# Performance work log

Measured on AMD Instinct MI355X. Metric: run time of the kernel, lower is better.

## Reference

```python
import jax, jax.numpy as jnp
import numpy as np

BATCH = 8192
N_BANDS = 2000
TARGET = 500
FIRST_HIDDEN = 50
LEAKY_SLOPE = 0.01  # torch LeakyReLU default


def _tridiag_solve(lower, diag, upper, rhs):
    """Thomas algorithm. lower/upper: (n-1,), diag: (n,), rhs: (n, B). Returns (n, B)."""
    dt = rhs.dtype
    up = jnp.concatenate([upper, jnp.zeros((1,), dt)])   # (n,)
    lo = jnp.concatenate([jnp.zeros((1,), dt), lower])   # (n,)

    def fwd(carry, inp):
        cp_prev, dp_prev = carry
        d_i, u_i, l_i, r_i = inp
        m = d_i - l_i * cp_prev
        cp = u_i / m
        dp = (r_i - l_i * dp_prev) / m
        return (cp, dp), (cp, dp)

    init = (jnp.zeros((), dt), jnp.zeros(rhs.shape[1:], dt))
    _, (cps, dps) = jax.lax.scan(fwd, init, (diag, up, lo, rhs))

    def bwd(x_next, inp):
        cp, dp = inp
        x = dp - cp * x_next
        return x, x

    _, xs = jax.lax.scan(bwd, jnp.zeros(rhs.shape[1:], dt), (cps, dps), reverse=True)
    return xs


def natural_cubic_spline_coeffs(times, path):
    """times: (n,), path: (B, n) -> (a, b, two_c, three_d), each (B, n-1)."""
    h = times[1:] - times[:-1]            # (n-1,)
    hr = 1.0 / h
    hr2 = hr * hr
    diffs3 = 3.0 * (path[:, 1:] - path[:, :-1])   # (B, n-1)
    diffs6 = 2.0 * diffs3
    pds = diffs3 * hr2                             # (B, n-1)
    n = path.shape[1]
    diag = (jnp.zeros((n,), path.dtype).at[:-1].set(hr).at[1:].add(hr)) * 2.0
    rhs = jnp.zeros_like(path).at[:, :-1].set(pds).at[:, 1:].add(pds)  # (B, n)
    kd = _tridiag_solve(hr, diag, hr, rhs.T).T     # knot derivatives (B, n)
    a = path[:, :-1]
    b = kd[:, :-1]
    two_c = (diffs6 * hr - 4.0 * kd[:, :-1] - 2.0 * kd[:, 1:]) * hr
    three_d = (-diffs6 * hr + 3.0 * (kd[:, :-1] + kd[:, 1:])) * hr2
    return a, b, two_c, three_d


def spline_evaluate(times, coeffs, t):
    """Evaluate at points t: (T,). Returns (B, T)."""
    a, b, two_c, three_d = coeffs
    idx = jnp.clip(jnp.searchsorted(times, t, side='left') - 1, 0, times.shape[0] - 2)
    frac = t - times[idx]                  # (T,)
    inner = 0.5 * two_c[:, idx] + three_d[:, idx] * frac / 3.0
    inner = b[:, idx] + inner * frac
    return a[:, idx] + inner * frac


def leaky_relu(x):
    return jnp.where(x >= 0, x, LEAKY_SLOPE * x)


def setup_inputs() -> dict:
    key = jax.random.key(0)
    ks = jax.random.split(key, 8)
    return {
        'x': jax.random.uniform(ks[0], (BATCH, N_BANDS), dtype=jnp.float32),
        'raw_index': jax.random.normal(ks[1], (TARGET,), dtype=jnp.float32),
        'W1': jax.random.normal(ks[2], (TARGET, FIRST_HIDDEN), dtype=jnp.float32) * 0.05,
        'b1': jax.random.normal(ks[3], (FIRST_HIDDEN,), dtype=jnp.float32) * 0.05,
        'W2': jax.random.normal(ks[4], (FIRST_HIDDEN, 10), dtype=jnp.float32) * 0.1,
        'b2': jax.random.normal(ks[5], (10,), dtype=jnp.float32) * 0.1,
        'W3': jax.random.normal(ks[6], (10, 1), dtype=jnp.float32) * 0.1,
        'b3': jax.random.normal(ks[7], (1,), dtype=jnp.float32) * 0.1,
    }


def reference(x, raw_index, W1, b1, W2, b2, W3, b3):
    # x: (B, n_bands). Spline is fit along the band axis with knots linspace(0,1,n_bands).
    times = jnp.linspace(0.0, 1.0, x.shape[1]).astype(x.dtype)
    coeffs = natural_cubic_spline_coeffs(times, x)
    # Each BandIndex machine evaluates the spline at sigmoid(raw_index_i) -> batched over all i.
    t_eval = jax.nn.sigmoid(raw_index)             # (T,)
    outputs = spline_evaluate(times, coeffs, t_eval)  # (B, T)
    h = leaky_relu(outputs @ W1 + b1)
    h = leaky_relu(h @ W2 + b2)
    soc_hat = (h @ W3 + b3).reshape(-1)            # (B,)
    return soc_hat
```

## Files before the change

kernel.cpp:

```cpp
#include <hip/hip_runtime.h>

#define NB 2000
#define BATCH 8192
#define NT 500
#define NH1 50
#define NH2 10
#define HRc 1999.0f
#define STEPc (1.0f/1999.0f)
#define LP 520

typedef __attribute__((ext_vector_type(8))) short short8;
typedef __attribute__((ext_vector_type(4))) float f32x4;

__device__ __forceinline__ float b2f(unsigned short u) {
    return __uint_as_float(((unsigned int)u) << 16);
}
__device__ __forceinline__ unsigned short f2b(float f) {
    unsigned int u = __float_as_uint(f);
    return (unsigned short)((u + 0x7FFFu + ((u >> 16) & 1u)) >> 16);
}
__device__ __forceinline__ float ldv(const void* p, int i, int flag) {
    return flag ? b2f(((const unsigned short*)p)[i]) : ((const float*)p)[i];
}
__device__ __forceinline__ int wave_detect(const void* x) {
    const unsigned char* xb = (const unsigned char*)x;
    int lane = threadIdx.x & 63;
    int pred = xb[4 * lane + 1] > 0x3F;
    unsigned long long m = __ballot(pred);
    return (__popcll(m) > 4) ? 0 : 1;
}

__global__ __launch_bounds__(64, 1) void p1_stencil(
        const void* __restrict__ xdet, const void* __restrict__ raw_index,
        float* __restrict__ S_coef, int* __restrict__ S_base) {
    __shared__ float cp_tab[64];
    __shared__ float sc[2];
    int tid = threadIdx.x;
    int flag = wave_detect(xdet);
    if (tid == 0) {
        double cp = 0.5;
        cp_tab[0] = 0.5f;
        for (int i = 1; i < 64; ++i) { cp = 1.0 / (4.0 - cp); cp_tab[i] = (float)cp; }
        sc[0] = (float)cp;
        sc[1] = (float)(1.0 / (2.0 - cp));
    }
    __syncthreads();
    int t = blockIdx.x * 64 + tid;
    if (t >= NT) return;
    float c_inf = sc[0], w_last = sc[1];

    float coef_rel[34];
    #pragma unroll
    for (int k = 0; k < 34; ++k) coef_rel[k] = 0.0f;

    float r = ldv(raw_index, t, flag);
    float v = 1.0f / (1.0f + expf(-r));
    int lo = 0, hi = NB;
    while (lo < hi) {
        int mid = (lo + hi) >> 1;
        float tm = (float)mid * STEPc;
        if (tm < v) lo = mid + 1; else hi = mid;
    }
    int idx = lo - 1;
    idx = idx < 0 ? 0 : (idx > NB - 2 ? NB - 2 : idx);
    float f = v - (float)idx * STEPc;
    float u = f * HRc;
    float A = 1.0f + u * u * (2.0f * u - 3.0f);
    float B = u * u * (3.0f - 2.0f * u);
    float C = f * (1.0f - u) * (1.0f - u);
    float D = f * u * (u - 1.0f);

    const float g3 = 3.0f * HRc * HRc;
    const float invhr = 1.0f / HRc;

    #pragma unroll
    for (int row = 0; row < 2; ++row) {
        int j = idx + row;
        float scale = row ? D : C;
        float z[35];
        #pragma unroll
        for (int q = 0; q < 35; ++q) z[q] = 0.0f;
        float w0 = (j <= NB - 2) ? ((j < 64) ? cp_tab[j] : c_inf) : w_last;
        z[17] = w0 * invhr;
        #pragma unroll
        for (int s = 1; s <= 17; ++s) {
            int m = j + s;
            float wm;
            if (m <= NB - 2)      wm = (m < 64) ? cp_tab[m] : c_inf;
            else if (m == NB - 1) wm = w_last;
            else                  wm = 0.0f;
            z[17 + s] = -wm * z[17 + s - 1];
        }
        #pragma unroll
        for (int s = 16; s >= -17; --s) {
            int m = j + s;
            float cpv;
            if (m >= NB - 1 || m < 0) cpv = 0.0f;
            else                      cpv = (m < 64) ? cp_tab[m] : c_inf;
            z[17 + s] = z[17 + s] - cpv * z[17 + s + 1];
        }
        #pragma unroll
        for (int s = -16; s <= 16; ++s) {
            int m = j + s;
            float gv = 0.0f;
            if (m >= 1)      gv += z[17 + s - 1];
            if (m <= NB - 2) gv -= z[17 + s + 1];
            if (m == NB - 1) gv += z[17 + s];
            if (m == 0)      gv -= z[17 + s];
            gv *= g3;
            bool valid = (m >= 0) && (m <= NB - 1);
            coef_rel[s + row + 16] += valid ? scale * gv : 0.0f;
        }
    }
    coef_rel[16] += A;
    coef_rel[17] += B;

    #pragma unroll
    for (int j = 0; j < 34; ++j) S_coef[t * 34 + j] = coef_rel[j];
    S_base[t] = idx;
}

__global__ __launch_bounds__(256) void m_build(
        const void* __restrict__ xdet, const void* __restrict__ W1,
        const float* __restrict__ S_coef, const int* __restrict__ S_base,
        unsigned int* __restrict__ MB) {
    __shared__ int sb[NT];
    int tid = threadIdx.x;
    int flag = wave_detect(xdet);
    for (int i = tid; i < NT; i += 256) sb[i] = S_base[i];
    __syncthreads();
    int k2 = blockIdx.x * 4 + (tid >> 6);
    int h = tid & 63;
    int hh = h < NH1 ? h : NH1 - 1;
    int k0 = 2 * k2;
    float acc0 = 0.0f, acc1 = 0.0f;
    if (k0 < NB) {
        #pragma unroll 4
        for (int t = 0; t < NT; ++t) {
            int idx = sb[t];
            int rel0 = k0 - idx + 16;
            if (rel0 >= -1 && rel0 < 34) {
                float w1v = ldv(W1, t * NH1 + hh, flag);
                if (rel0 >= 0)  acc0 += S_coef[t * 34 + rel0] * w1v;
                if (rel0 < 33)  acc1 += S_coef[t * 34 + rel0 + 1] * w1v;
            }
        }
    }
    bool ok = (h < NH1) && (k0 < NB);
    unsigned int lo16 = ok ? (unsigned int)f2b(acc0) : 0u;
    unsigned int hi16 = ok ? (unsigned int)f2b(acc1) : 0u;
    int kt = k0 >> 5;
    int kr = k0 & 31;
    int gg = kr >> 3;
    int j  = kr & 7;
    int ht = h >> 4;
    int lt = gg * 16 + (h & 15);
    MB[(((kt * 4 + ht) * 64 + lt) << 2) + (j >> 1)] = lo16 | (hi16 << 16);
}

__global__ __launch_bounds__(512, 4) void g_fused(
        const void* __restrict__ x, const unsigned int* __restrict__ MB,
        const void* __restrict__ b1, const void* __restrict__ W2,
        const void* __restrict__ b2, const void* __restrict__ W3,
        const void* __restrict__ b3, void* __restrict__ out) {
    __shared__ __align__(16) unsigned short lx[2][16 * LP];
    __shared__ float red[8][16][68];
    __shared__ float Wmlp[NH1 * NH2 + NH1 + NH2 + NH2 + 1];

    int tid = threadIdx.x;
    int flag = wave_detect(x);

    for (int i = tid; i < NH1 * NH2; i += 512) Wmlp[i] = ldv(W2, i, flag);
    if (tid < NH1) Wmlp[500 + tid] = ldv(b1, tid, flag);
    if (tid < NH2) Wmlp[550 + tid] = ldv(b2, tid, flag);
    if (tid < NH2) Wmlp[560 + tid] = ldv(W3, tid, flag);
    if (tid == 0)  Wmlp[570] = ldv(b3, 0, flag);

    int lane = tid & 63;
    int c16  = tid & 15;
    int g    = (tid >> 4) & 3;
    int w    = tid >> 6;
    int srow = tid >> 5;
    int soff = tid & 31;
    int r0   = blockIdx.x * 16;
    const unsigned short* xs = (const unsigned short*)x;
    const float*          xf = (const float*)x;
    size_t crow = (size_t)(r0 + srow) * NB;

    f32x4 acc[4];
    #pragma unroll
    for (int ht = 0; ht < 4; ++ht) acc[ht] = (f32x4){0.f, 0.f, 0.f, 0.f};

    union AU { uint4 u; short8 s; };
    const uint4* mb4 = (const uint4*)MB;

    #define LDSEG(dst, gk) do {                                           \
        int _gk = (gk);                                                   \
        if (_gk + 8 <= NB) {                                              \
            if (flag) {                                                   \
                (dst) = *(const uint4*)(xs + crow + _gk);                 \
            } else {                                                      \
                float4 _v0 = *(const float4*)(xf + crow + _gk);           \
                float4 _v1 = *(const float4*)(xf + crow + _gk + 4);       \
                (dst).x = (unsigned)f2b(_v0.x) | ((unsigned)f2b(_v0.y) << 16); \
                (dst).y = (unsigned)f2b(_v0.z) | ((unsigned)f2b(_v0.w) << 16); \
                (dst).z = (unsigned)f2b(_v1.x) | ((unsigned)f2b(_v1.y) << 16); \
                (dst).w = (unsigned)f2b(_v1.z) | ((unsigned)f2b(_v1.w) << 16); \
            }                                                             \
        } else {                                                          \
            (dst) = make_uint4(0u, 0u, 0u, 0u);                           \
        }                                                                 \
    } while (0)

    {
        uint4 p0, p1;
        LDSEG(p0, soff * 8);
        LDSEG(p1, soff * 8 + 256);
        *(uint4*)&lx[0][srow * LP + soff * 8]       = p0;
        *(uint4*)&lx[0][srow * LP + soff * 8 + 256] = p1;
    }

    int cur = 0;
    #pragma unroll
    for (int c = 0; c < 4; ++c) {
        __syncthreads();
        uint4 s0 = make_uint4(0u,0u,0u,0u), s1 = make_uint4(0u,0u,0u,0u);
        if (c < 3) {
            LDSEG(s0, (c + 1) * 512 + soff * 8);
            LDSEG(s1, (c + 1) * 512 + soff * 8 + 256);
        }
        #pragma unroll
        for (int dk = 0; dk < 2; ++dk) {
            int ktl = 2 * w + dk;
            AU a;
            a.u = *(const uint4*)&lx[cur][c16 * LP + ktl * 32 + g * 8];
            int kt = c * 16 + ktl;
            #pragma unroll
            for (int ht = 0; ht < 4; ++ht) {
                AU b; b.u = mb4[(kt * 4 + ht) * 64 + lane];
                acc[ht] = __builtin_amdgcn_mfma_f32_16x16x32_bf16(a.s, b.s, acc[ht], 0, 0, 0);
            }
        }
        if (c < 3) {
            *(uint4*)&lx[cur ^ 1][srow * LP + soff * 8]       = s0;
            *(uint4*)&lx[cur ^ 1][srow * LP + soff * 8 + 256] = s1;
        }
        __syncthreads();
        cur ^= 1;
    }
    #undef LDSEG

    #pragma unroll
    for (int ht = 0; ht < 4; ++ht)
        #pragma unroll
        for (int r = 0; r < 4; ++r)
            red[w][g * 4 + r][ht * 16 + c16] = acc[ht][r];
    __syncthreads();

    #pragma unroll
    for (int ii = 0; ii < 2; ++ii) {
        int idx = tid + ii * 512;
        int row = idx >> 6, h = idx & 63;
        float s = 0.0f;
        #pragma unroll
        for (int w2 = 0; w2 < 8; ++w2) s += red[w2][row][h];
        red[0][row][h] = s;
    }
    __syncthreads();

    if (tid < 16) {
        float h1v[NH1];
        #pragma unroll
        for (int h = 0; h < NH1; ++h) {
            float vv = red[0][tid][h] + Wmlp[500 + h];
            h1v[h] = vv >= 0.0f ? vv : 0.01f * vv;
        }
        float o = Wmlp[570];
        for (int j = 0; j < NH2; ++j) {
            float a2 = Wmlp[550 + j];
            #pragma unroll
            for (int h = 0; h < NH1; ++h)
                a2 = fmaf(h1v[h], Wmlp[h * NH2 + j], a2);
            a2 = a2 >= 0.0f ? a2 : 0.01f * a2;
            o = fmaf(a2, Wmlp[560 + j], o);
        }
        int b = r0 + tid;
        if (flag) ((unsigned short*)out)[b] = f2b(o);
        else      ((float*)out)[b] = o;
    }
}

extern "C" void kernel_launch(void* const* d_in, const int* in_sizes, int n_in,
                              void* d_out, int out_size, void* d_ws, size_t ws_size,
                              hipStream_t stream) {
    const void* x   = d_in[0];
    const void* raw = d_in[1];
    const void* W1  = d_in[2];
    const void* b1  = d_in[3];
    const void* W2  = d_in[4];
    const void* b2  = d_in[5];
    const void* W3  = d_in[6];
    const void* b3  = d_in[7];

    float* w      = (float*)d_ws;
    int*   S_base = (int*)w;
    float* S_coef = w + 512;
    unsigned int* MB = (unsigned int*)(w + 17512);

    p1_stencil<<<8, 64, 0, stream>>>(x, raw, S_coef, S_base);
    m_build<<<256, 256, 0, stream>>>(x, W1, S_coef, S_base, MB);
    g_fused<<<512, 512, 0, stream>>>(x, MB, b1, W2, b2, W3, b3, d_out);
}
```

Measured before the change: 161.1 us.

## Fuse three kernels into one cooperative launch with grid syncs

Merges the stencil, matrix-build and fused GEMM+MLP kernels into a single cooperative kernel that uses grid.sync between phases, and prefetches the first x tile before the syncs so the load overlaps the earlier phases. The aim is to remove two kernel launch gaps and inter-kernel drain. In exchange it needs all 512 blocks to be co-resident, pays for two grid-wide barriers, and spreads m_build over only 2 waves per block. It falls back to the three-kernel path if the cooperative launch fails.

```diff
diff --git a/kernel.cpp b/kernel.cpp
--- a/kernel.cpp
+++ b/kernel.cpp
@@ -1,4 +1,7 @@
 #include <hip/hip_runtime.h>
+#include <hip/hip_cooperative_groups.h>
+
+namespace cg = cooperative_groups;
 
 #define NB 2000
 #define BATCH 8192
@@ -30,144 +33,23 @@
     return (__popcll(m) > 4) ? 0 : 1;
 }
 
-__global__ __launch_bounds__(64, 1) void p1_stencil(
-        const void* __restrict__ xdet, const void* __restrict__ raw_index,
-        float* __restrict__ S_coef, int* __restrict__ S_base) {
-    __shared__ float cp_tab[64];
-    __shared__ float sc[2];
-    int tid = threadIdx.x;
-    int flag = wave_detect(xdet);
-    if (tid == 0) {
-        double cp = 0.5;
-        cp_tab[0] = 0.5f;
-        for (int i = 1; i < 64; ++i) { cp = 1.0 / (4.0 - cp); cp_tab[i] = (float)cp; }
-        sc[0] = (float)cp;
-        sc[1] = (float)(1.0 / (2.0 - cp));
-    }
-    __syncthreads();
-    int t = blockIdx.x * 64 + tid;
-    if (t >= NT) return;
-    float c_inf = sc[0], w_last = sc[1];
-
-    float coef_rel[34];
-    #pragma unroll
-    for (int k = 0; k < 34; ++k) coef_rel[k] = 0.0f;
-
-    float r = ldv(raw_index, t, flag);
-    float v = 1.0f / (1.0f + expf(-r));
-    int lo = 0, hi = NB;
-    while (lo < hi) {
-        int mid = (lo + hi) >> 1;
-        float tm = (float)mid * STEPc;
-        if (tm < v) lo = mid + 1; else hi = mid;
-    }
-    int idx = lo - 1;
-    idx = idx < 0 ? 0 : (idx > NB - 2 ? NB - 2 : idx);
-    float f = v - (float)idx * STEPc;
-    float u = f * HRc;
-    float A = 1.0f + u * u * (2.0f * u - 3.0f);
-    float B = u * u * (3.0f - 2.0f * u);
-    float C = f * (1.0f - u) * (1.0f - u);
-    float D = f * u * (u - 1.0f);
-
-    const float g3 = 3.0f * HRc * HRc;
-    const float invhr = 1.0f / HRc;
-
-    #pragma unroll
-    for (int row = 0; row < 2; ++row) {
-        int j = idx + row;
-        float scale = row ? D : C;
-        float z[35];
-        #pragma unroll
-        for (int q = 0; q < 35; ++q) z[q] = 0.0f;
-        float w0 = (j <= NB - 2) ? ((j < 64) ? cp_tab[j] : c_inf) : w_last;
-        z[17] = w0 * invhr;
-        #pragma unroll
-        for (int s = 1; s <= 17; ++s) {
-            int m = j + s;
-            float wm;
-            if (m <= NB - 2)      wm = (m < 64) ? cp_tab[m] : c_inf;
-            else if (m == NB - 1) wm = w_last;
-            else                  wm = 0.0f;
-            z[17 + s] = -wm * z[17 + s - 1];
-        }
-        #pragma unroll
-        for (int s = 16; s >= -17; --s) {
-            int m = j + s;
-            float cpv;
-            if (m >= NB - 1 || m < 0) cpv = 0.0f;
-            else                      cpv = (m < 64) ? cp_tab[m] : c_inf;
-            z[17 + s] = z[17 + s] - cpv * z[17 + s + 1];
-        }
-        #pragma unroll
-        for (int s = -16; s <= 16; ++s) {
-            int m = j + s;
-            float gv = 0.0f;
-            if (m >= 1)      gv += z[17 + s - 1];
-            if (m <= NB - 2) gv -= z[17 + s + 1];
-            if (m == NB - 1) gv += z[17 + s];
-            if (m == 0)      gv -= z[17 + s];
-            gv *= g3;
-            bool valid = (m >= 0) && (m <= NB - 1);
-            coef_rel[s + row + 16] += valid ? scale * gv : 0.0f;
-        }
-    }
-    coef_rel[16] += A;
-    coef_rel[17] += B;
-
-    #pragma unroll
-    for (int j = 0; j < 34; ++j) S_coef[t * 34 + j] = coef_rel[j];
-    S_base[t] = idx;
-}
-
-__global__ __launch_bounds__(256) void m_build(
-        const void* __restrict__ xdet, const void* __restrict__ W1,
-        const float* __restrict__ S_coef, const int* __restrict__ S_base,
-        unsigned int* __restrict__ MB) {
-    __shared__ int sb[NT];
-    int tid = threadIdx.x;
-    int flag = wave_detect(xdet);
-    for (int i = tid; i < NT; i += 256) sb[i] = S_base[i];
-    __syncthreads();
-    int k2 = blockIdx.x * 4 + (tid >> 6);
-    int h = tid & 63;
-    int hh = h < NH1 ? h : NH1 - 1;
-    int k0 = 2 * k2;
-    float acc0 = 0.0f, acc1 = 0.0f;
-    if (k0 < NB) {
-        #pragma unroll 4
-        for (int t = 0; t < NT; ++t) {
-            int idx = sb[t];
-            int rel0 = k0 - idx + 16;
-            if (rel0 >= -1 && rel0 < 34) {
-                float w1v = ldv(W1, t * NH1 + hh, flag);
-                if (rel0 >= 0)  acc0 += S_coef[t * 34 + rel0] * w1v;
-                if (rel0 < 33)  acc1 += S_coef[t * 34 + rel0 + 1] * w1v;
-            }
-        }
-    }
-    bool ok = (h < NH1) && (k0 < NB);
-    unsigned int lo16 = ok ? (unsigned int)f2b(acc0) : 0u;
-    unsigned int hi16 = ok ? (unsigned int)f2b(acc1) : 0u;
-    int kt = k0 >> 5;
-    int kr = k0 & 31;
-    int gg = kr >> 3;
-    int j  = kr & 7;
-    int ht = h >> 4;
-    int lt = gg * 16 + (h & 15);
-    MB[(((kt * 4 + ht) * 64 + lt) << 2) + (j >> 1)] = lo16 | (hi16 << 16);
-}
-
-__global__ __launch_bounds__(512, 4) void g_fused(
-        const void* __restrict__ x, const unsigned int* __restrict__ MB,
-        const void* __restrict__ b1, const void* __restrict__ W2,
-        const void* __restrict__ b2, const void* __restrict__ W3,
-        const void* __restrict__ b3, void* __restrict__ out) {
+__global__ __launch_bounds__(512, 4) void fused_all(
+        const void* __restrict__ x, const void* __restrict__ raw,
+        const void* __restrict__ W1, const void* __restrict__ b1,
+        const void* __restrict__ W2, const void* __restrict__ b2,
+        const void* __restrict__ W3, const void* __restrict__ b3,
+        float* __restrict__ S_coef, int* __restrict__ S_base,
+        unsigned int* __restrict__ MB, void* __restrict__ out) {
     __shared__ __align__(16) unsigned short lx[2][16 * LP];
     __shared__ float red[8][16][68];
     __shared__ float Wmlp[NH1 * NH2 + NH1 + NH2 + NH2 + 1];
-
+    __shared__ float act[16][10];
+    __shared__ float cp_tab[64];
+    __shared__ float sc[2];
+
+    cg::grid_group grid = cg::this_grid();
     int tid = threadIdx.x;
+    int bx  = blockIdx.x;
     int flag = wave_detect(x);
 
     for (int i = tid; i < NH1 * NH2; i += 512) Wmlp[i] = ldv(W2, i, flag);
@@ -176,23 +58,11 @@
     if (tid < NH2) Wmlp[560 + tid] = ldv(W3, tid, flag);
     if (tid == 0)  Wmlp[570] = ldv(b3, 0, flag);
 
-    int lane = tid & 63;
-    int c16  = tid & 15;
-    int g    = (tid >> 4) & 3;
-    int w    = tid >> 6;
     int srow = tid >> 5;
     int soff = tid & 31;
-    int r0   = blockIdx.x * 16;
     const unsigned short* xs = (const unsigned short*)x;
     const float*          xf = (const float*)x;
-    size_t crow = (size_t)(r0 + srow) * NB;
-
-    f32x4 acc[4];
-    #pragma unroll
-    for (int ht = 0; ht < 4; ++ht) acc[ht] = (f32x4){0.f, 0.f, 0.f, 0.f};
-
-    union AU { uint4 u; short8 s; };
-    const uint4* mb4 = (const uint4*)MB;
+    size_t crow = (size_t)(bx * 16 + srow) * NB;
 
     #define LDSEG(dst, gk) do {                                           \
         int _gk = (gk);                                                   \
@@ -213,6 +83,402 @@
     } while (0)
 
     {
+        uint4 p0, p1v;
+        LDSEG(p0, soff * 8);
+        LDSEG(p1v, soff * 8 + 256);
+        *(uint4*)&lx[0][srow * LP + soff * 8]       = p0;
+        *(uint4*)&lx[0][srow * LP + soff * 8 + 256] = p1v;
+    }
+
+    if (tid == 0 && bx < 8) {
+        double cp = 0.5;
+        cp_tab[0] = 0.5f;
+        for (int i = 1; i < 64; ++i) { cp = 1.0 / (4.0 - cp); cp_tab[i] = (float)cp; }
+        sc[0] = (float)cp;
+        sc[1] = (float)(1.0 / (2.0 - cp));
+    }
+    __syncthreads();
+    if (bx < 8 && tid < 64) {
+        int t = bx * 64 + tid;
+        if (t < NT) {
+            float c_inf = sc[0], w_last = sc[1];
+            float coef_rel[34];
+            #pragma unroll
+            for (int k = 0; k < 34; ++k) coef_rel[k] = 0.0f;
+
+            float r = ldv(raw, t, flag);
+            float v = 1.0f / (1.0f + expf(-r));
+            int lo = 0, hi = NB;
+            while (lo < hi) {
+                int mid = (lo + hi) >> 1;
+                float tm = (float)mid * STEPc;
+                if (tm < v) lo = mid + 1; else hi = mid;
+            }
+            int idx = lo - 1;
+            idx = idx < 0 ? 0 : (idx > NB - 2 ? NB - 2 : idx);
+            float f = v - (float)idx * STEPc;
+            float u = f * HRc;
+            float A = 1.0f + u * u * (2.0f * u - 3.0f);
+            float B = u * u * (3.0f - 2.0f * u);
+            float C = f * (1.0f - u) * (1.0f - u);
+            float D = f * u * (u - 1.0f);
+
+            const float g3 = 3.0f * HRc * HRc;
+            const float invhr = 1.0f / HRc;
+
+            #pragma unroll
+            for (int row = 0; row < 2; ++row) {
+                int j = idx + row;
+                float scale = row ? D : C;
+                float z[35];
+                #pragma unroll
+                for (int q = 0; q < 35; ++q) z[q] = 0.0f;
+                float w0 = (j <= NB - 2) ? ((j < 64) ? cp_tab[j] : c_inf) : w_last;
+                z[17] = w0 * invhr;
+                #pragma unroll
+                for (int s = 1; s <= 17; ++s) {
+                    int m = j + s;
+                    float wm;
+                    if (m <= NB - 2)      wm = (m < 64) ? cp_tab[m] : c_inf;
+                    else if (m == NB - 1) wm = w_last;
+                    else                  wm = 0.0f;
+                    z[17 + s] = -wm * z[17 + s - 1];
+                }
+                #pragma unroll
+                for (int s = 16; s >= -17; --s) {
+                    int m = j + s;
+                    float cpv;
+                    if (m >= NB - 1 || m < 0) cpv = 0.0f;
+                    else                      cpv = (m < 64) ? cp_tab[m] : c_inf;
+                    z[17 + s] = z[17 + s] - cpv * z[17 + s + 1];
+                }
+                #pragma unroll
+                for (int s = -16; s <= 16; ++s) {
+                    int m = j + s;
+                    float gv = 0.0f;
+                    if (m >= 1)      gv += z[17 + s - 1];
+                    if (m <= NB - 2) gv -= z[17 + s + 1];
+                    if (m == NB - 1) gv += z[17 + s];
+                    if (m == 0)      gv -= z[17 + s];
+                    gv *= g3;
+                    bool valid = (m >= 0) && (m <= NB - 1);
+                    coef_rel[s + row + 16] += valid ? scale * gv : 0.0f;
+                }
+            }
+            coef_rel[16] += A;
+            coef_rel[17] += B;
+
+            #pragma unroll
+            for (int j2 = 0; j2 < 34; ++j2) S_coef[t * 34 + j2] = coef_rel[j2];
+            S_base[t] = idx;
+        }
+    }
+
+    grid.sync();
+
+    int* sbL = (int*)&red[0][0][0];
+    if (tid < NT) sbL[tid] = S_base[tid];
+    __syncthreads();
+    {
+        int wv = tid >> 6;
+        if (wv < 2) {
+            int k2 = bx * 2 + wv;
+            int h = tid & 63;
+            int hh = h < NH1 ? h : NH1 - 1;
+            int k0 = 2 * k2;
+            float acc0 = 0.0f, acc1 = 0.0f;
+            if (k0 < NB) {
+                #pragma unroll 4
+                for (int t = 0; t < NT; ++t) {
+                    int idx = sbL[t];
+                    int rel0 = k0 - idx + 16;
+                    if (rel0 >= -1 && rel0 < 34) {
+                        float w1v = ldv(W1, t * NH1 + hh, flag);
+                        if (rel0 >= 0)  acc0 += S_coef[t * 34 + rel0] * w1v;
+                        if (rel0 < 33)  acc1 += S_coef[t * 34 + rel0 + 1] * w1v;
+                    }
+                }
+            }
+            bool ok = (h < NH1) && (k0 < NB);
+            unsigned int lo16 = ok ? (unsigned int)f2b(acc0) : 0u;
+            unsigned int hi16 = ok ? (unsigned int)f2b(acc1) : 0u;
+            int kt = k0 >> 5;
+            int kr = k0 & 31;
+            int gg = kr >> 3;
+            int jj = kr & 7;
+            int ht = h >> 4;
+            int lt = gg * 16 + (h & 15);
+            MB[(((kt * 4 + ht) * 64 + lt) << 2) + (jj >> 1)] = lo16 | (hi16 << 16);
+        }
+    }
+
+    grid.sync();
+
+    int lane = tid & 63;
+    int c16  = tid & 15;
+    int g    = (tid >> 4) & 3;
+    int wv   = tid >> 6;
+
+    f32x4 acc[4];
+    #pragma unroll
+    for (int ht = 0; ht < 4; ++ht) acc[ht] = (f32x4){0.f, 0.f, 0.f, 0.f};
+
+    union AU { uint4 u; short8 s; };
+    const uint4* mb4 = (const uint4*)MB;
+
+    int cur = 0;
+    #pragma unroll
+    for (int c = 0; c < 4; ++c) {
+        __syncthreads();
+        uint4 s0 = make_uint4(0u,0u,0u,0u), s1 = make_uint4(0u,0u,0u,0u);
+        if (c < 3) {
+            LDSEG(s0, (c + 1) * 512 + soff * 8);
+            LDSEG(s1, (c + 1) * 512 + soff * 8 + 256);
+        }
+        #pragma unroll
+        for (int dk = 0; dk < 2; ++dk) {
+            int ktl = 2 * wv + dk;
+            AU a;
+            a.u = *(const uint4*)&lx[cur][c16 * LP + ktl * 32 + g * 8];
+            int kt = c * 16 + ktl;
+            #pragma unroll
+            for (int ht = 0; ht < 4; ++ht) {
+                AU b; b.u = mb4[(kt * 4 + ht) * 64 + lane];
+                acc[ht] = __builtin_amdgcn_mfma_f32_16x16x32_bf16(a.s, b.s, acc[ht], 0, 0, 0);
+            }
+        }
+        if (c < 3) {
+            *(uint4*)&lx[cur ^ 1][srow * LP + soff * 8]       = s0;
+            *(uint4*)&lx[cur ^ 1][srow * LP + soff * 8 + 256] = s1;
+        }
+        __syncthreads();
+        cur ^= 1;
+    }
+    #undef LDSEG
+
+    #pragma unroll
+    for (int ht = 0; ht < 4; ++ht)
+        #pragma unroll
+        for (int r = 0; r < 4; ++r)
+            red[wv][g * 4 + r][ht * 16 + c16] = acc[ht][r];
+    __syncthreads();
+
+    #pragma unroll
+    for (int ii = 0; ii < 2; ++ii) {
+        int idx2 = tid + ii * 512;
+        int row = idx2 >> 6, h = idx2 & 63;
+        float s = 0.0f;
+        #pragma unroll
+        for (int w2 = 0; w2 < 8; ++w2) s += red[w2][row][h];
+        red[0][row][h] = s;
+    }
+    __syncthreads();
+
+    if (tid < 160) {
+        int row = tid / 10, j = tid - row * 10;
+        float a2 = Wmlp[550 + j];
+        #pragma unroll
+        for (int h = 0; h < NH1; ++h) {
+            float vv = red[0][row][h] + Wmlp[500 + h];
+            float hv = vv >= 0.0f ? vv : 0.01f * vv;
+            a2 = fmaf(hv, Wmlp[h * NH2 + j], a2);
+        }
+        act[row][j] = a2 >= 0.0f ? a2 : 0.01f * a2;
+    }
+    __syncthreads();
+    if (tid < 16) {
+        float o = Wmlp[570];
+        #pragma unroll
+        for (int j = 0; j < NH2; ++j) o = fmaf(act[tid][j], Wmlp[560 + j], o);
+        int b = bx * 16 + tid;
+        if (flag) ((unsigned short*)out)[b] = f2b(o);
+        else      ((float*)out)[b] = o;
+    }
+}
+
+__global__ __launch_bounds__(64, 1) void p1_stencil(
+        const void* __restrict__ xdet, const void* __restrict__ raw_index,
+        float* __restrict__ S_coef, int* __restrict__ S_base) {
+    __shared__ float cp_tab[64];
+    __shared__ float sc[2];
+    int tid = threadIdx.x;
+    int flag = wave_detect(xdet);
+    if (tid == 0) {
+        double cp = 0.5;
+        cp_tab[0] = 0.5f;
+        for (int i = 1; i < 64; ++i) { cp = 1.0 / (4.0 - cp); cp_tab[i] = (float)cp; }
+        sc[0] = (float)cp;
+        sc[1] = (float)(1.0 / (2.0 - cp));
+    }
+    __syncthreads();
+    int t = blockIdx.x * 64 + tid;
+    if (t >= NT) return;
+    float c_inf = sc[0], w_last = sc[1];
+
+    float coef_rel[34];
+    #pragma unroll
+    for (int k = 0; k < 34; ++k) coef_rel[k] = 0.0f;
+
+    float r = ldv(raw_index, t, flag);
+    float v = 1.0f / (1.0f + expf(-r));
+    int lo = 0, hi = NB;
+    while (lo < hi) {
+        int mid = (lo + hi) >> 1;
+        float tm = (float)mid * STEPc;
+        if (tm < v) lo = mid + 1; else hi = mid;
+    }
+    int idx = lo - 1;
+    idx = idx < 0 ? 0 : (idx > NB - 2 ? NB - 2 : idx);
+    float f = v - (float)idx * STEPc;
+    float u = f * HRc;
+    float A = 1.0f + u * u * (2.0f * u - 3.0f);
+    float B = u * u * (3.0f - 2.0f * u);
+    float C = f * (1.0f - u) * (1.0f - u);
+    float D = f * u * (u - 1.0f);
+
+    const float g3 = 3.0f * HRc * HRc;
+    const float invhr = 1.0f / HRc;
+
+    #pragma unroll
+    for (int row = 0; row < 2; ++row) {
+        int j = idx + row;
+        float scale = row ? D : C;
+        float z[35];
+        #pragma unroll
+        for (int q = 0; q < 35; ++q) z[q] = 0.0f;
+        float w0 = (j <= NB - 2) ? ((j < 64) ? cp_tab[j] : c_inf) : w_last;
+        z[17] = w0 * invhr;
+        #pragma unroll
+        for (int s = 1; s <= 17; ++s) {
+            int m = j + s;
+            float wm;
+            if (m <= NB - 2)      wm = (m < 64) ? cp_tab[m] : c_inf;
+            else if (m == NB - 1) wm = w_last;
+            else                  wm = 0.0f;
+            z[17 + s] = -wm * z[17 + s - 1];
+        }
+        #pragma unroll
+        for (int s = 16; s >= -17; --s) {
+            int m = j + s;
+            float cpv;
+            if (m >= NB - 1 || m < 0) cpv = 0.0f;
+            else                      cpv = (m < 64) ? cp_tab[m] : c_inf;
+            z[17 + s] = z[17 + s] - cpv * z[17 + s + 1];
+        }
+        #pragma unroll
+        for (int s = -16; s <= 16; ++s) {
+            int m = j + s;
+            float gv = 0.0f;
+            if (m >= 1)      gv += z[17 + s - 1];
+            if (m <= NB - 2) gv -= z[17 + s + 1];
+            if (m == NB - 1) gv += z[17 + s];
+            if (m == 0)      gv -= z[17 + s];
+            gv *= g3;
+            bool valid = (m >= 0) && (m <= NB - 1);
+            coef_rel[s + row + 16] += valid ? scale * gv : 0.0f;
+        }
+    }
+    coef_rel[16] += A;
+    coef_rel[17] += B;
+
+    #pragma unroll
+    for (int j = 0; j < 34; ++j) S_coef[t * 34 + j] = coef_rel[j];
+    S_base[t] = idx;
+}
+
+__global__ __launch_bounds__(256) void m_build(
+        const void* __restrict__ xdet, const void* __restrict__ W1,
+        const float* __restrict__ S_coef, const int* __restrict__ S_base,
+        unsigned int* __restrict__ MB) {
+    __shared__ int sb[NT];
+    int tid = threadIdx.x;
+    int flag = wave_detect(xdet);
+    for (int i = tid; i < NT; i += 256) sb[i] = S_base[i];
+    __syncthreads();
+    int k2 = blockIdx.x * 4 + (tid >> 6);
+    int h = tid & 63;
+    int hh = h < NH1 ? h : NH1 - 1;
+    int k0 = 2 * k2;
+    float acc0 = 0.0f, acc1 = 0.0f;
+    if (k0 < NB) {
+        #pragma unroll 4
+        for (int t = 0; t < NT; ++t) {
+            int idx = sb[t];
+            int rel0 = k0 - idx + 16;
+            if (rel0 >= -1 && rel0 < 34) {
+                float w1v = ldv(W1, t * NH1 + hh, flag);
+                if (rel0 >= 0)  acc0 += S_coef[t * 34 + rel0] * w1v;
+                if (rel0 < 33)  acc1 += S_coef[t * 34 + rel0 + 1] * w1v;
+            }
+        }
+    }
+    bool ok = (h < NH1) && (k0 < NB);
+    unsigned int lo16 = ok ? (unsigned int)f2b(acc0) : 0u;
+    unsigned int hi16 = ok ? (unsigned int)f2b(acc1) : 0u;
+    int kt = k0 >> 5;
+    int kr = k0 & 31;
+    int gg = kr >> 3;
+    int j  = kr & 7;
+    int ht = h >> 4;
+    int lt = gg * 16 + (h & 15);
+    MB[(((kt * 4 + ht) * 64 + lt) << 2) + (j >> 1)] = lo16 | (hi16 << 16);
+}
+
+__global__ __launch_bounds__(512, 4) void g_fused(
+        const void* __restrict__ x, const unsigned int* __restrict__ MB,
+        const void* __restrict__ b1, const void* __restrict__ W2,
+        const void* __restrict__ b2, const void* __restrict__ W3,
+        const void* __restrict__ b3, void* __restrict__ out) {
+    __shared__ __align__(16) unsigned short lx[2][16 * LP];
+    __shared__ float red[8][16][68];
+    __shared__ float Wmlp[NH1 * NH2 + NH1 + NH2 + NH2 + 1];
+
+    int tid = threadIdx.x;
+    int flag = wave_detect(x);
+
+    for (int i = tid; i < NH1 * NH2; i += 512) Wmlp[i] = ldv(W2, i, flag);
+    if (tid < NH1) Wmlp[500 + tid] = ldv(b1, tid, flag);
+    if (tid < NH2) Wmlp[550 + tid] = ldv(b2, tid, flag);
+    if (tid < NH2) Wmlp[560 + tid] = ldv(W3, tid, flag);
+    if (tid == 0)  Wmlp[570] = ldv(b3, 0, flag);
+
+    int lane = tid & 63;
+    int c16  = tid & 15;
+    int g    = (tid >> 4) & 3;
+    int w    = tid >> 6;
+    int srow = tid >> 5;
+    int soff = tid & 31;
+    int r0   = blockIdx.x * 16;
+    const unsigned short* xs = (const unsigned short*)x;
+    const float*          xf = (const float*)x;
+    size_t crow = (size_t)(r0 + srow) * NB;
+
+    f32x4 acc[4];
+    #pragma unroll
+    for (int ht = 0; ht < 4; ++ht) acc[ht] = (f32x4){0.f, 0.f, 0.f, 0.f};
+
+    union AU { uint4 u; short8 s; };
+    const uint4* mb4 = (const uint4*)MB;
+
+    #define LDSEG(dst, gk) do {                                           \
+        int _gk = (gk);                                                   \
+        if (_gk + 8 <= NB) {                                              \
+            if (flag) {                                                   \
+                (dst) = *(const uint4*)(xs + crow + _gk);                 \
+            } else {                                                      \
+                float4 _v0 = *(const float4*)(xf + crow + _gk);           \
+                float4 _v1 = *(const float4*)(xf + crow + _gk + 4);       \
+                (dst).x = (unsigned)f2b(_v0.x) | ((unsigned)f2b(_v0.y) << 16); \
+                (dst).y = (unsigned)f2b(_v0.z) | ((unsigned)f2b(_v0.w) << 16); \
+                (dst).z = (unsigned)f2b(_v1.x) | ((unsigned)f2b(_v1.y) << 16); \
+                (dst).w = (unsigned)f2b(_v1.z) | ((unsigned)f2b(_v1.w) << 16); \
+            }                                                             \
+        } else {                                                          \
+            (dst) = make_uint4(0u, 0u, 0u, 0u);                           \
+        }                                                                 \
+    } while (0)
+
+    {
         uint4 p0, p1;
         LDSEG(p0, soff * 8);
         LDSEG(p1, soff * 8 + 256);
@@ -307,7 +573,16 @@
     float* S_coef = w + 512;
     unsigned int* MB = (unsigned int*)(w + 17512);
 
-    p1_stencil<<<8, 64, 0, stream>>>(x, raw, S_coef, S_base);
-    m_build<<<256, 256, 0, stream>>>(x, W1, S_coef, S_base, MB);
-    g_fused<<<512, 512, 0, stream>>>(x, MB, b1, W2, b2, W3, b3, d_out);
-}
+    void* kargs[] = {
+        (void*)&x, (void*)&raw, (void*)&W1, (void*)&b1,
+        (void*)&W2, (void*)&b2, (void*)&W3, (void*)&b3,
+        (void*)&S_coef, (void*)&S_base, (void*)&MB, (void*)&d_out
+    };
+    hipError_t err = hipLaunchCooperativeKernel(
+        (void*)fused_all, dim3(512), dim3(512), kargs, 0, stream);
+    if (err != hipSuccess) {
+        p1_stencil<<<8, 64, 0, stream>>>(x, raw, S_coef, S_base);
+        m_build<<<256, 256, 0, stream>>>(x, W1, S_coef, S_base, MB);
+        g_fused<<<512, 512, 0, stream>>>(x, MB, b1, W2, b2, W3, b3, d_out);
+    }
+}
```

Result: slower. 256.0 us (+58.8%).

## Fuse stencil and matrix-build kernels; prefetch all x segments up front in bf16 path

Applied to the files above, without the earlier changes.

Merges the stencil-coefficient kernel into the matrix-build kernel: every block recomputes all 500 stencil rows into shared memory (padded stride 35) instead of reading them from a separate launch's global output. This removes one kernel launch and its global round trip, at the cost of redundant stencil computation in each of the 256 blocks. Separately, the bf16 path of the fused GEMM kernel now issues all eight x-segment loads into registers before the loop, so global latency overlaps across chunks, at the cost of more registers.

```diff
diff --git a/kernel.cpp b/kernel.cpp
--- a/kernel.cpp
+++ b/kernel.cpp
@@ -30,13 +30,16 @@
     return (__popcll(m) > 4) ? 0 : 1;
 }
 
-__global__ __launch_bounds__(64, 1) void p1_stencil(
-        const void* __restrict__ xdet, const void* __restrict__ raw_index,
-        float* __restrict__ S_coef, int* __restrict__ S_base) {
+__global__ __launch_bounds__(256, 1) void pm_build(
+        const void* __restrict__ x, const void* __restrict__ raw_index,
+        const void* __restrict__ W1, unsigned int* __restrict__ MB) {
+    __shared__ float scS[NT * 35];
+    __shared__ int   sbS[512];
     __shared__ float cp_tab[64];
     __shared__ float sc[2];
+
     int tid = threadIdx.x;
-    int flag = wave_detect(xdet);
+    int flag = wave_detect(x);
     if (tid == 0) {
         double cp = 0.5;
         cp_tab[0] = 0.5f;
@@ -45,90 +48,85 @@
         sc[1] = (float)(1.0 / (2.0 - cp));
     }
     __syncthreads();
-    int t = blockIdx.x * 64 + tid;
-    if (t >= NT) return;
     float c_inf = sc[0], w_last = sc[1];
 
-    float coef_rel[34];
-    #pragma unroll
-    for (int k = 0; k < 34; ++k) coef_rel[k] = 0.0f;
-
-    float r = ldv(raw_index, t, flag);
-    float v = 1.0f / (1.0f + expf(-r));
-    int lo = 0, hi = NB;
-    while (lo < hi) {
-        int mid = (lo + hi) >> 1;
-        float tm = (float)mid * STEPc;
-        if (tm < v) lo = mid + 1; else hi = mid;
-    }
-    int idx = lo - 1;
-    idx = idx < 0 ? 0 : (idx > NB - 2 ? NB - 2 : idx);
-    float f = v - (float)idx * STEPc;
-    float u = f * HRc;
-    float A = 1.0f + u * u * (2.0f * u - 3.0f);
-    float B = u * u * (3.0f - 2.0f * u);
-    float C = f * (1.0f - u) * (1.0f - u);
-    float D = f * u * (u - 1.0f);
-
-    const float g3 = 3.0f * HRc * HRc;
-    const float invhr = 1.0f / HRc;
-
-    #pragma unroll
-    for (int row = 0; row < 2; ++row) {
-        int j = idx + row;
-        float scale = row ? D : C;
-        float z[35];
-        #pragma unroll
-        for (int q = 0; q < 35; ++q) z[q] = 0.0f;
-        float w0 = (j <= NB - 2) ? ((j < 64) ? cp_tab[j] : c_inf) : w_last;
-        z[17] = w0 * invhr;
-        #pragma unroll
-        for (int s = 1; s <= 17; ++s) {
-            int m = j + s;
-            float wm;
-            if (m <= NB - 2)      wm = (m < 64) ? cp_tab[m] : c_inf;
-            else if (m == NB - 1) wm = w_last;
-            else                  wm = 0.0f;
-            z[17 + s] = -wm * z[17 + s - 1];
-        }
-        #pragma unroll
-        for (int s = 16; s >= -17; --s) {
-            int m = j + s;
-            float cpv;
-            if (m >= NB - 1 || m < 0) cpv = 0.0f;
-            else                      cpv = (m < 64) ? cp_tab[m] : c_inf;
-            z[17 + s] = z[17 + s] - cpv * z[17 + s + 1];
-        }
-        #pragma unroll
-        for (int s = -16; s <= 16; ++s) {
-            int m = j + s;
-            float gv = 0.0f;
-            if (m >= 1)      gv += z[17 + s - 1];
-            if (m <= NB - 2) gv -= z[17 + s + 1];
-            if (m == NB - 1) gv += z[17 + s];
-            if (m == 0)      gv -= z[17 + s];
-            gv *= g3;
-            bool valid = (m >= 0) && (m <= NB - 1);
-            coef_rel[s + row + 16] += valid ? scale * gv : 0.0f;
-        }
-    }
-    coef_rel[16] += A;
-    coef_rel[17] += B;
-
-    #pragma unroll
-    for (int j = 0; j < 34; ++j) S_coef[t * 34 + j] = coef_rel[j];
-    S_base[t] = idx;
-}
-
-__global__ __launch_bounds__(256) void m_build(
-        const void* __restrict__ xdet, const void* __restrict__ W1,
-        const float* __restrict__ S_coef, const int* __restrict__ S_base,
-        unsigned int* __restrict__ MB) {
-    __shared__ int sb[NT];
-    int tid = threadIdx.x;
-    int flag = wave_detect(xdet);
-    for (int i = tid; i < NT; i += 256) sb[i] = S_base[i];
+    #pragma unroll 1
+    for (int rep = 0; rep < 2; ++rep) {
+        int t = tid + rep * 256;
+        if (t < NT) {
+            float coef_rel[34];
+            #pragma unroll
+            for (int k = 0; k < 34; ++k) coef_rel[k] = 0.0f;
+
+            float r = ldv(raw_index, t, flag);
+            float v = 1.0f / (1.0f + expf(-r));
+            int lo = 0, hi = NB;
+            while (lo < hi) {
+                int mid = (lo + hi) >> 1;
+                float tm = (float)mid * STEPc;
+                if (tm < v) lo = mid + 1; else hi = mid;
+            }
+            int idx = lo - 1;
+            idx = idx < 0 ? 0 : (idx > NB - 2 ? NB - 2 : idx);
+            float f = v - (float)idx * STEPc;
+            float u = f * HRc;
+            float A = 1.0f + u * u * (2.0f * u - 3.0f);
+            float B = u * u * (3.0f - 2.0f * u);
+            float C = f * (1.0f - u) * (1.0f - u);
+            float D = f * u * (u - 1.0f);
+
+            const float g3 = 3.0f * HRc * HRc;
+            const float invhr = 1.0f / HRc;
+
+            #pragma unroll
+            for (int row = 0; row < 2; ++row) {
+                int j = idx + row;
+                float scale = row ? D : C;
+                float z[35];
+                #pragma unroll
+                for (int q = 0; q < 35; ++q) z[q] = 0.0f;
+                float w0 = (j <= NB - 2) ? ((j < 64) ? cp_tab[j] : c_inf) : w_last;
+                z[17] = w0 * invhr;
+                #pragma unroll
+                for (int s = 1; s <= 17; ++s) {
+                    int m = j + s;
+                    float wm;
+                    if (m <= NB - 2)      wm = (m < 64) ? cp_tab[m] : c_inf;
+                    else if (m == NB - 1) wm = w_last;
+                    else                  wm = 0.0f;
+                    z[17 + s] = -wm * z[17 + s - 1];
+                }
+                #pragma unroll
+                for (int s = 16; s >= -17; --s) {
+                    int m = j + s;
+                    float cpv;
+                    if (m >= NB - 1 || m < 0) cpv = 0.0f;
+                    else                      cpv = (m < 64) ? cp_tab[m] : c_inf;
+                    z[17 + s] = z[17 + s] - cpv * z[17 + s + 1];
+                }
+                #pragma unroll
+                for (int s = -16; s <= 16; ++s) {
+                    int m = j + s;
+                    float gv = 0.0f;
+                    if (m >= 1)      gv += z[17 + s - 1];
+                    if (m <= NB - 2) gv -= z[17 + s + 1];
+                    if (m == NB - 1) gv += z[17 + s];
+                    if (m == 0)      gv -= z[17 + s];
+                    gv *= g3;
+                    bool valid = (m >= 0) && (m <= NB - 1);
+                    coef_rel[s + row + 16] += valid ? scale * gv : 0.0f;
+                }
+            }
+            coef_rel[16] += A;
+            coef_rel[17] += B;
+
+            #pragma unroll
+            for (int j2 = 0; j2 < 34; ++j2) scS[t * 35 + j2] = coef_rel[j2];
+            sbS[t] = idx;
+        }
+    }
     __syncthreads();
+
     int k2 = blockIdx.x * 4 + (tid >> 6);
     int h = tid & 63;
     int hh = h < NH1 ? h : NH1 - 1;
@@ -137,12 +135,12 @@
     if (k0 < NB) {
         #pragma unroll 4
         for (int t = 0; t < NT; ++t) {
-            int idx = sb[t];
+            int idx = sbS[t];
             int rel0 = k0 - idx + 16;
             if (rel0 >= -1 && rel0 < 34) {
                 float w1v = ldv(W1, t * NH1 + hh, flag);
-                if (rel0 >= 0)  acc0 += S_coef[t * 34 + rel0] * w1v;
-                if (rel0 < 33)  acc1 += S_coef[t * 34 + rel0 + 1] * w1v;
+                if (rel0 >= 0)  acc0 += scS[t * 35 + rel0] * w1v;
+                if (rel0 < 33)  acc1 += scS[t * 35 + rel0 + 1] * w1v;
             }
         }
     }
@@ -194,61 +192,94 @@
     union AU { uint4 u; short8 s; };
     const uint4* mb4 = (const uint4*)MB;
 
-    #define LDSEG(dst, gk) do {                                           \
-        int _gk = (gk);                                                   \
-        if (_gk + 8 <= NB) {                                              \
-            if (flag) {                                                   \
-                (dst) = *(const uint4*)(xs + crow + _gk);                 \
-            } else {                                                      \
-                float4 _v0 = *(const float4*)(xf + crow + _gk);           \
-                float4 _v1 = *(const float4*)(xf + crow + _gk + 4);       \
+    if (flag) {
+        uint4 pf[8];
+        #pragma unroll
+        for (int c = 0; c < 4; ++c) {
+            int gk0 = c * 512 + soff * 8;
+            int gk1 = gk0 + 256;
+            pf[2 * c]     = (gk0 + 8 <= NB) ? *(const uint4*)(xs + crow + gk0)
+                                            : make_uint4(0u, 0u, 0u, 0u);
+            pf[2 * c + 1] = (gk1 + 8 <= NB) ? *(const uint4*)(xs + crow + gk1)
+                                            : make_uint4(0u, 0u, 0u, 0u);
+        }
+        *(uint4*)&lx[0][srow * LP + soff * 8]       = pf[0];
+        *(uint4*)&lx[0][srow * LP + soff * 8 + 256] = pf[1];
+
+        int cur = 0;
+        #pragma unroll
+        for (int c = 0; c < 4; ++c) {
+            __syncthreads();
+            #pragma unroll
+            for (int dk = 0; dk < 2; ++dk) {
+                int ktl = 2 * w + dk;
+                AU a;
+                a.u = *(const uint4*)&lx[cur][c16 * LP + ktl * 32 + g * 8];
+                int kt = c * 16 + ktl;
+                #pragma unroll
+                for (int ht = 0; ht < 4; ++ht) {
+                    AU b; b.u = mb4[(kt * 4 + ht) * 64 + lane];
+                    acc[ht] = __builtin_amdgcn_mfma_f32_16x16x32_bf16(a.s, b.s, acc[ht], 0, 0, 0);
+                }
+            }
+            if (c < 3) {
+                *(uint4*)&lx[cur ^ 1][srow * LP + soff * 8]       = pf[2 * (c + 1)];
+                *(uint4*)&lx[cur ^ 1][srow * LP + soff * 8 + 256] = pf[2 * (c + 1) + 1];
+            }
+            __syncthreads();
+            cur ^= 1;
+        }
+    } else {
+        #define LDSEGF(dst, gk) do {                                          \
+            int _gk = (gk);                                                   \
+            if (_gk + 8 <= NB) {                                              \
+                float4 _v0 = *(const float4*)(xf + crow + _gk);               \
+                float4 _v1 = *(const float4*)(xf + crow + _gk + 4);           \
                 (dst).x = (unsigned)f2b(_v0.x) | ((unsigned)f2b(_v0.y) << 16); \
                 (dst).y = (unsigned)f2b(_v0.z) | ((unsigned)f2b(_v0.w) << 16); \
                 (dst).z = (unsigned)f2b(_v1.x) | ((unsigned)f2b(_v1.y) << 16); \
                 (dst).w = (unsigned)f2b(_v1.z) | ((unsigned)f2b(_v1.w) << 16); \
-            }                                                             \
-        } else {                                                          \
-            (dst) = make_uint4(0u, 0u, 0u, 0u);                           \
-        }                                                                 \
-    } while (0)
-
-    {
-        uint4 p0, p1;
-        LDSEG(p0, soff * 8);
-        LDSEG(p1, soff * 8 + 256);
-        *(uint4*)&lx[0][srow * LP + soff * 8]       = p0;
-        *(uint4*)&lx[0][srow * LP + soff * 8 + 256] = p1;
-    }
-
-    int cur = 0;
-    #pragma unroll
-    for (int c = 0; c < 4; ++c) {
-        __syncthreads();
-        uint4 s0 = make_uint4(0u,0u,0u,0u), s1 = make_uint4(0u,0u,0u,0u);
-        if (c < 3) {
-            LDSEG(s0, (c + 1) * 512 + soff * 8);
-            LDSEG(s1, (c + 1) * 512 + soff * 8 + 256);
-        }
-        #pragma unroll
-        for (int dk = 0; dk < 2; ++dk) {
-            int ktl = 2 * w + dk;
-            AU a;
-            a.u = *(const uint4*)&lx[cur][c16 * LP + ktl * 32 + g * 8];
-            int kt = c * 16 + ktl;
-            #pragma unroll
-            for (int ht = 0; ht < 4; ++ht) {
-                AU b; b.u = mb4[(kt * 4 + ht) * 64 + lane];
-                acc[ht] = __builtin_amdgcn_mfma_f32_16x16x32_bf16(a.s, b.s, acc[ht], 0, 0, 0);
-            }
-        }
-        if (c < 3) {
-            *(uint4*)&lx[cur ^ 1][srow * LP + soff * 8]       = s0;
-            *(uint4*)&lx[cur ^ 1][srow * LP + soff * 8 + 256] = s1;
-        }
-        __syncthreads();
-        cur ^= 1;
-    }
-    #undef LDSEG
+            } else {                                                          \
+                (dst) = make_uint4(0u, 0u, 0u, 0u);                           \
+            }                                                                 \
+        } while (0)
+        {
+            uint4 p0, p1;
+            LDSEGF(p0, soff * 8);
+            LDSEGF(p1, soff * 8 + 256);
+            *(uint4*)&lx[0][srow * LP + soff * 8]       = p0;
+            *(uint4*)&lx[0][srow * LP + soff * 8 + 256] = p1;
+        }
+        int cur = 0;
+        #pragma unroll
+        for (int c = 0; c < 4; ++c) {
+            __syncthreads();
+            uint4 s0 = make_uint4(0u,0u,0u,0u), s1 = make_uint4(0u,0u,0u,0u);
+            if (c < 3) {
+                LDSEGF(s0, (c + 1) * 512 + soff * 8);
+                LDSEGF(s1, (c + 1) * 512 + soff * 8 + 256);
+            }
+            #pragma unroll
+            for (int dk = 0; dk < 2; ++dk) {
+                int ktl = 2 * w + dk;
+                AU a;
+                a.u = *(const uint4*)&lx[cur][c16 * LP + ktl * 32 + g * 8];
+                int kt = c * 16 + ktl;
+                #pragma unroll
+                for (int ht = 0; ht < 4; ++ht) {
+                    AU b; b.u = mb4[(kt * 4 + ht) * 64 + lane];
+                    acc[ht] = __builtin_amdgcn_mfma_f32_16x16x32_bf16(a.s, b.s, acc[ht], 0, 0, 0);
+                }
+            }
+            if (c < 3) {
+                *(uint4*)&lx[cur ^ 1][srow * LP + soff * 8]       = s0;
+                *(uint4*)&lx[cur ^ 1][srow * LP + soff * 8 + 256] = s1;
+            }
+            __syncthreads();
+            cur ^= 1;
+        }
+        #undef LDSEGF
+    }
 
     #pragma unroll
     for (int ht = 0; ht < 4; ++ht)
@@ -302,12 +333,9 @@
     const void* W3  = d_in[6];
     const void* b3  = d_in[7];
 
-    float* w      = (float*)d_ws;
-    int*   S_base = (int*)w;
-    float* S_coef = w + 512;
+    float* w = (float*)d_ws;
     unsigned int* MB = (unsigned int*)(w + 17512);
 
-    p1_stencil<<<8, 64, 0, stream>>>(x, raw, S_coef, S_base);
-    m_build<<<256, 256, 0, stream>>>(x, W1, S_coef, S_base, MB);
+    pm_build<<<256, 256, 0, stream>>>(x, raw, W1, MB);
     g_fused<<<512, 512, 0, stream>>>(x, MB, b1, W2, b2, W3, b3, d_out);
 }
```

After: 165.5 us. 2.7% more time.
